# Kernel tuning notes

Measured on AMD Instinct MI355X. Metric: run time of the kernel, lower is better.

## Reference

```python
import jax, jax.numpy as jnp
import numpy as np

DK, DL, HID = 128, 128, 128  # per init_kwargs: mlp_list=[256,128,128]


def setup_inputs() -> dict:
    key = jax.random.key(0)
    k1, k2, k3, k4, k5 = jax.random.split(key, 5)
    B, K, L = 2, 128, 4096
    inputA = jax.random.normal(k1, (B, K, DK), dtype=jnp.float32)
    inputB = jax.random.normal(k2, (B, L, DL), dtype=jnp.float32)
    # MLP layer 0: Linear(256 -> 128), kaiming-uniform-ish init
    lim1 = 1.0 / np.sqrt(DK + DL)
    W1 = jax.random.uniform(k3, (DK + DL, HID), jnp.float32, -lim1, lim1)
    b1 = jax.random.uniform(k4, (HID,), jnp.float32, -lim1, lim1)
    # scoring Linear(128 -> 1, bias=False)
    lim2 = 1.0 / np.sqrt(HID)
    w2 = jax.random.uniform(k5, (HID,), jnp.float32, -lim2, lim2)
    return {"inputA": inputA, "inputB": inputB, "W1": W1, "b1": b1,
            "w2": w2, "nA": K, "nB": L}


def reference(inputA, inputB, W1, b1, w2, nA, nB):
    # Original: tC = cat([repeat(A), repeat(B)], -1); mlp(tC); linear; softmax(L).
    # Fused-equivalent math: split W1 rows between the A-part and B-part of the
    # concat, so the first Linear is two small matmuls + broadcast add.
    hA = jnp.einsum('bkd,dh->bkh', inputA, W1[:DK])        # (B, K, H)
    hB = jnp.einsum('bld,dh->blh', inputB, W1[DK:])        # (B, L, H)
    h = jax.nn.relu(hA[:, :, None, :] + hB[:, None, :, :] + b1)  # (B, K, L, H)
    scores = jnp.einsum('bklh,h->bkl', h, w2)              # (B, K, L)
    return jax.nn.softmax(scores, axis=2)
```

## Files before the change

### kernel.cpp

```cpp
#include <hip/hip_runtime.h>
#include <hip/hip_fp16.h>
#include <math.h>

constexpr int BB = 2;
constexpr int KK = 128;
constexpr int LL = 4096;
constexpr int DD = 128;
constexpr int HH = 128;

__device__ __forceinline__ float4 ld4(const float* p) {
    return *reinterpret_cast<const float4*>(p);
}

__device__ __forceinline__ __half2 hmax2(__half2 a, __half2 b) {
    unsigned ua = __builtin_bit_cast(unsigned, a);
    unsigned ub = __builtin_bit_cast(unsigned, b);
    unsigned ud;
    asm("v_pk_max_f16 %0, %1, %2" : "=v"(ud) : "v"(ua), "v"(ub));
    return __builtin_bit_cast(__half2, ud);
}

__device__ __forceinline__ uint32_t duph(float x) {
    __half h = __float2half(x);
    unsigned short us = __builtin_bit_cast(unsigned short, h);
    return (uint32_t)us * 0x10001u;
}

__global__ __launch_bounds__(256) void k1_gemm(
    const float* __restrict__ inA, const float* __restrict__ inB,
    const float* __restrict__ W1, const float* __restrict__ b1,
    const float* __restrict__ w2,
    uint32_t* __restrict__ u_dup, uint32_t* __restrict__ w2_dup,
    __half* __restrict__ vT)
{
    __shared__ __align__(16) char smem[49 * 1024];
    float*  sIn = reinterpret_cast<float*>(smem);
    float4* sW4 = reinterpret_cast<float4*>(smem + 16 * 1024);
    float*  sT  = reinterpret_cast<float*>(smem + 16 * 1024);

    const int bid = blockIdx.x;
    const int tid = threadIdx.x;

    int row0;
    bool isA;
    if (bid < 256) {
        const int x = bid & 7, y = bid >> 3;
        const int C = x + 8 * (y & 1);
        row0 = C * 512 + (y >> 1) * 32;
        isA = false;
    } else {
        row0 = (bid - 256) * 32;
        isA = true;
    }
    const float* src = (isA ? inA : inB) + (size_t)row0 * DD;
    const float4* wsrc = reinterpret_cast<const float4*>(W1 + (isA ? 0 : DD * HH));

    #pragma unroll
    for (int j = 0; j < 4; ++j) {
        const int idx = tid + 256 * j;
        reinterpret_cast<float4*>(sIn)[idx] =
            reinterpret_cast<const float4*>(src)[idx];
    }

    const int tx = tid & 31;
    const int ty = tid >> 5;

    float accx[4], accy[4], accz[4], accw[4];
    #pragma unroll
    for (int r = 0; r < 4; ++r) { accx[r] = accy[r] = accz[r] = accw[r] = 0.f; }

    for (int wh = 0; wh < 2; ++wh) {
        __syncthreads();
        #pragma unroll
        for (int q = 0; q < 8; ++q)
            sW4[tid + 256 * q] = wsrc[wh * 2048 + tid + 256 * q];
        __syncthreads();

        #pragma unroll 2
        for (int dd0 = 0; dd0 < 64; dd0 += 4) {
            const int d0 = wh * 64 + dd0;
            float4 w4[4];
            #pragma unroll
            for (int dd = 0; dd < 4; ++dd)
                w4[dd] = sW4[(dd0 + dd) * 32 + tx];
            float a[4][4];
            #pragma unroll
            for (int r = 0; r < 4; ++r) {
                float4 a4 = ld4(&sIn[(ty * 4 + r) * 128 + d0]);
                a[r][0] = a4.x; a[r][1] = a4.y; a[r][2] = a4.z; a[r][3] = a4.w;
            }
            #pragma unroll
            for (int dd = 0; dd < 4; ++dd) {
                const float4 wv = w4[dd];
                #pragma unroll
                for (int r = 0; r < 4; ++r) {
                    const float av = a[r][dd];
                    accx[r] = fmaf(av, wv.x, accx[r]);
                    accy[r] = fmaf(av, wv.y, accy[r]);
                    accz[r] = fmaf(av, wv.z, accz[r]);
                    accw[r] = fmaf(av, wv.w, accw[r]);
                }
            }
        }
    }

    if (isA) {
        const float4 bb = ld4(&b1[tx * 4]);
        #pragma unroll
        for (int r = 0; r < 4; ++r) {
            uint4 o;
            o.x = duph(accx[r] + bb.x);
            o.y = duph(accy[r] + bb.y);
            o.z = duph(accz[r] + bb.z);
            o.w = duph(accw[r] + bb.w);
            *reinterpret_cast<uint4*>(
                &u_dup[(size_t)(row0 + ty * 4 + r) * HH + tx * 4]) = o;
        }
        if (bid == 256 && tid < HH) w2_dup[tid] = duph(w2[tid]);
    } else {
        __syncthreads();
        #pragma unroll
        for (int r = 0; r < 4; ++r) {
            const int l = ty * 4 + r;
            sT[(tx * 4 + 0) * 33 + l] = accx[r];
            sT[(tx * 4 + 1) * 33 + l] = accy[r];
            sT[(tx * 4 + 2) * 33 + l] = accz[r];
            sT[(tx * 4 + 3) * 33 + l] = accw[r];
        }
        __syncthreads();
        const int h    = tid >> 1;
        const int half = tid & 1;
        const int bsel = row0 >> 12;
        const int l0   = (row0 & 4095) + half * 16;
        uint32_t o[8];
        #pragma unroll
        for (int i = 0; i < 8; ++i) {
            const float lo = sT[h * 33 + half * 16 + 2 * i];
            const float hi = sT[h * 33 + half * 16 + 2 * i + 1];
            o[i] = __builtin_bit_cast(uint32_t, __floats2half2_rn(lo, hi));
        }
        uint32_t* dst = reinterpret_cast<uint32_t*>(vT) +
                        (size_t)(bsel * HH + h) * (LL / 2) + l0 / 2;
        uint4 s0; s0.x = o[0]; s0.y = o[1]; s0.z = o[2]; s0.w = o[3];
        uint4 s1; s1.x = o[4]; s1.y = o[5]; s1.z = o[6]; s1.w = o[7];
        *reinterpret_cast<uint4*>(dst)     = s0;
        *reinterpret_cast<uint4*>(dst + 4) = s1;
    }
}

__global__ __launch_bounds__(512) void k2_score(
    const uint32_t* __restrict__ u_dup, const uint32_t* __restrict__ w2_dup,
    const __half* __restrict__ vT, float* __restrict__ out)
{
    __shared__ __align__(16) uint32_t sU[8 * HH];
    __shared__ __align__(16) uint32_t sW[HH];

    int m = blockIdx.x;
    const int cb = m & 7;   m >>= 3;
    const int kt = m & 15;  m >>= 4;
    const int b  = m;
    const int tid = threadIdx.x;

    if (tid < 256)
        reinterpret_cast<uint4*>(sU)[tid] =
            reinterpret_cast<const uint4*>(u_dup + (size_t)(b * KK + kt * 8) * HH)[tid];
    else if (tid < 288)
        reinterpret_cast<uint4*>(sW)[tid - 256] =
            reinterpret_cast<const uint4*>(w2_dup)[tid - 256];
    __syncthreads();

    const int kh = tid >> 8;
    const int t  = tid & 255;
    const int p  = cb * 256 + t;
    const uint32_t* vp = reinterpret_cast<const uint32_t*>(vT)
                         + (size_t)b * HH * (LL / 2) + p;
    const uint32_t* su = sU + kh * 4 * HH;

    const __half2 hz = __float2half2_rn(0.f);
    float2 facc[4];
    #pragma unroll
    for (int k = 0; k < 4; ++k) { facc[k].x = 0.f; facc[k].y = 0.f; }

    for (int g = 0; g < 8; ++g) {
        const int h0 = g * 16;
        uint32_t v[16];
        #pragma unroll
        for (int jj = 0; jj < 16; ++jj)
            v[jj] = vp[(size_t)(h0 + jj) * (LL / 2)];

        __half2 acc[4];
        #pragma unroll
        for (int k = 0; k < 4; ++k) acc[k] = hz;

        #pragma unroll
        for (int q = 0; q < 4; ++q) {
            const uint4 wc = *reinterpret_cast<const uint4*>(&sW[h0 + q * 4]);
            uint4 uc[4];
            #pragma unroll
            for (int k = 0; k < 4; ++k)
                uc[k] = *reinterpret_cast<const uint4*>(&su[k * HH + h0 + q * 4]);
            const uint32_t* wq = reinterpret_cast<const uint32_t*>(&wc);
            #pragma unroll
            for (int jj = 0; jj < 4; ++jj) {
                const __half2 ww = __builtin_bit_cast(__half2, wq[jj]);
                const __half2 vv = __builtin_bit_cast(__half2, v[q * 4 + jj]);
                #pragma unroll
                for (int k = 0; k < 4; ++k) {
                    const uint32_t* uq = reinterpret_cast<const uint32_t*>(&uc[k]);
                    __half2 tt = __hadd2(vv, __builtin_bit_cast(__half2, uq[jj]));
                    acc[k] = __hfma2(hmax2(tt, hz), ww, acc[k]);
                }
            }
        }
        #pragma unroll
        for (int k = 0; k < 4; ++k) {
            const float2 f = __half22float2(acc[k]);
            facc[k].x += f.x; facc[k].y += f.y;
        }
    }

    #pragma unroll
    for (int k = 0; k < 4; ++k)
        *reinterpret_cast<float2*>(
            &out[(size_t)(b * KK + kt * 8 + kh * 4 + k) * LL + 2 * p]) = facc[k];
}

__global__ __launch_bounds__(1024) void k3_softmax(float* __restrict__ out)
{
    __shared__ float reds[16];

    const int row = blockIdx.x;
    float* p = out + (size_t)row * LL;
    const int tid = threadIdx.x;

    float4 x = reinterpret_cast<const float4*>(p)[tid];

    x.x = expf(x.x); x.y = expf(x.y);
    x.z = expf(x.z); x.w = expf(x.w);
    float s = (x.x + x.y) + (x.z + x.w);
    #pragma unroll
    for (int off = 32; off > 0; off >>= 1)
        s += __shfl_xor(s, off, 64);
    const int lane = tid & 63, wv = tid >> 6;
    if (lane == 0) reds[wv] = s;
    __syncthreads();
    if (tid < 16) {
        float ss = reds[tid];
        #pragma unroll
        for (int off = 8; off > 0; off >>= 1)
            ss += __shfl_xor(ss, off, 64);
        reds[tid] = ss;
    }
    __syncthreads();
    s = reds[0];

    const float inv = 1.0f / s;
    x.x *= inv; x.y *= inv; x.z *= inv; x.w *= inv;
    reinterpret_cast<float4*>(p)[tid] = x;
}

extern "C" void kernel_launch(void* const* d_in, const int* in_sizes, int n_in,
                              void* d_out, int out_size, void* d_ws, size_t ws_size,
                              hipStream_t stream)
{
    const float* inA = (const float*)d_in[0];
    const float* inB = (const float*)d_in[1];
    const float* W1  = (const float*)d_in[2];
    const float* b1  = (const float*)d_in[3];
    const float* w2  = (const float*)d_in[4];
    float* out = (float*)d_out;

    char* ws = (char*)d_ws;
    uint32_t* u_dup  = (uint32_t*)ws;
    uint32_t* w2_dup = (uint32_t*)(ws + 0x20000);
    __half*   vT     = (__half*)(ws + 0x40000);

    hipLaunchKernelGGL(k1_gemm, dim3(264), dim3(256), 0, stream,
                       inA, inB, W1, b1, w2, u_dup, w2_dup, vT);
    hipLaunchKernelGGL(k2_score, dim3(256), dim3(512), 0, stream,
                       u_dup, w2_dup, vT, out);
    hipLaunchKernelGGL(k3_softmax, dim3(BB * KK), dim3(1024), 0, stream, out);
}
```

Measured before the change: 30.19 us.

## Pack hidden dim as half2 pairs and read per-thread hB rows

Changes the packed-half layout so each half2 holds two hidden channels instead of two L positions. hB is now stored row-major (L,H) in fp16 with no shared-memory transpose, and the duplicated u/w2 buffers become compact packed pairs. The score kernel gives each thread one L position and 8 K rows, loads its 256-byte hB row with vector loads, and reads u and w2 straight from global memory (uniform, likely scalar loads) instead of staging them in LDS. The aim is to drop the transpose and LDS traffic and halve the u/w2 footprint. In exchange, row-per-thread loads are strided across lanes, which may coalesce poorly, and the output stores become scalar.

```diff
diff --git a/kernel.cpp b/kernel.cpp
--- a/kernel.cpp
+++ b/kernel.cpp
@@ -20,23 +20,20 @@
     return __builtin_bit_cast(__half2, ud);
 }
 
-__device__ __forceinline__ uint32_t duph(float x) {
-    __half h = __float2half(x);
-    unsigned short us = __builtin_bit_cast(unsigned short, h);
-    return (uint32_t)us * 0x10001u;
+__device__ __forceinline__ uint32_t pkh2(float a, float b) {
+    return __builtin_bit_cast(uint32_t, __floats2half2_rn(a, b));
 }
 
 __global__ __launch_bounds__(256) void k1_gemm(
     const float* __restrict__ inA, const float* __restrict__ inB,
     const float* __restrict__ W1, const float* __restrict__ b1,
     const float* __restrict__ w2,
-    uint32_t* __restrict__ u_dup, uint32_t* __restrict__ w2_dup,
-    __half* __restrict__ vT)
-{
-    __shared__ __align__(16) char smem[49 * 1024];
+    uint32_t* __restrict__ u_pk, uint32_t* __restrict__ w2_pk,
+    __half* __restrict__ vh)
+{
+    __shared__ __align__(16) char smem[48 * 1024];
     float*  sIn = reinterpret_cast<float*>(smem);
     float4* sW4 = reinterpret_cast<float4*>(smem + 16 * 1024);
-    float*  sT  = reinterpret_cast<float*>(smem + 16 * 1024);
 
     const int bid = blockIdx.x;
     const int tid = threadIdx.x;
@@ -108,121 +105,80 @@
         const float4 bb = ld4(&b1[tx * 4]);
         #pragma unroll
         for (int r = 0; r < 4; ++r) {
-            uint4 o;
-            o.x = duph(accx[r] + bb.x);
-            o.y = duph(accy[r] + bb.y);
-            o.z = duph(accz[r] + bb.z);
-            o.w = duph(accw[r] + bb.w);
-            *reinterpret_cast<uint4*>(
-                &u_dup[(size_t)(row0 + ty * 4 + r) * HH + tx * 4]) = o;
-        }
-        if (bid == 256 && tid < HH) w2_dup[tid] = duph(w2[tid]);
+            uint2 o;
+            o.x = pkh2(accx[r] + bb.x, accy[r] + bb.y);
+            o.y = pkh2(accz[r] + bb.z, accw[r] + bb.w);
+            *reinterpret_cast<uint2*>(
+                &u_pk[(size_t)(row0 + ty * 4 + r) * 64 + tx * 2]) = o;
+        }
+        if (bid == 256 && tid < 64)
+            w2_pk[tid] = pkh2(w2[2 * tid], w2[2 * tid + 1]);
     } else {
-        __syncthreads();
+        const int bsel = row0 >> 12;
         #pragma unroll
         for (int r = 0; r < 4; ++r) {
-            const int l = ty * 4 + r;
-            sT[(tx * 4 + 0) * 33 + l] = accx[r];
-            sT[(tx * 4 + 1) * 33 + l] = accy[r];
-            sT[(tx * 4 + 2) * 33 + l] = accz[r];
-            sT[(tx * 4 + 3) * 33 + l] = accw[r];
-        }
-        __syncthreads();
-        const int h    = tid >> 1;
-        const int half = tid & 1;
-        const int bsel = row0 >> 12;
-        const int l0   = (row0 & 4095) + half * 16;
-        uint32_t o[8];
-        #pragma unroll
-        for (int i = 0; i < 8; ++i) {
-            const float lo = sT[h * 33 + half * 16 + 2 * i];
-            const float hi = sT[h * 33 + half * 16 + 2 * i + 1];
-            o[i] = __builtin_bit_cast(uint32_t, __floats2half2_rn(lo, hi));
-        }
-        uint32_t* dst = reinterpret_cast<uint32_t*>(vT) +
-                        (size_t)(bsel * HH + h) * (LL / 2) + l0 / 2;
-        uint4 s0; s0.x = o[0]; s0.y = o[1]; s0.z = o[2]; s0.w = o[3];
-        uint4 s1; s1.x = o[4]; s1.y = o[5]; s1.z = o[6]; s1.w = o[7];
-        *reinterpret_cast<uint4*>(dst)     = s0;
-        *reinterpret_cast<uint4*>(dst + 4) = s1;
+            const int lrow = (row0 & 4095) + ty * 4 + r;
+            uint2 o;
+            o.x = pkh2(accx[r], accy[r]);
+            o.y = pkh2(accz[r], accw[r]);
+            *reinterpret_cast<uint2*>(
+                &vh[((size_t)bsel * LL + lrow) * HH + tx * 4]) = o;
+        }
     }
 }
 
 __global__ __launch_bounds__(512) void k2_score(
-    const uint32_t* __restrict__ u_dup, const uint32_t* __restrict__ w2_dup,
-    const __half* __restrict__ vT, float* __restrict__ out)
-{
-    __shared__ __align__(16) uint32_t sU[8 * HH];
-    __shared__ __align__(16) uint32_t sW[HH];
-
+    const uint32_t* __restrict__ u_pk, const uint32_t* __restrict__ w2_pk,
+    const __half* __restrict__ vh, float* __restrict__ out)
+{
     int m = blockIdx.x;
     const int cb = m & 7;   m >>= 3;
     const int kt = m & 15;  m >>= 4;
     const int b  = m;
     const int tid = threadIdx.x;
 
-    if (tid < 256)
-        reinterpret_cast<uint4*>(sU)[tid] =
-            reinterpret_cast<const uint4*>(u_dup + (size_t)(b * KK + kt * 8) * HH)[tid];
-    else if (tid < 288)
-        reinterpret_cast<uint4*>(sW)[tid - 256] =
-            reinterpret_cast<const uint4*>(w2_dup)[tid - 256];
-    __syncthreads();
-
-    const int kh = tid >> 8;
-    const int t  = tid & 255;
-    const int p  = cb * 256 + t;
-    const uint32_t* vp = reinterpret_cast<const uint32_t*>(vT)
-                         + (size_t)b * HH * (LL / 2) + p;
-    const uint32_t* su = sU + kh * 4 * HH;
-
+    const int l = cb * 512 + tid;
+    const uint4* vrow = reinterpret_cast<const uint4*>(
+                            vh + ((size_t)b * LL + l) * HH);
+    const uint32_t* up = u_pk + (size_t)(b * KK + kt * 8) * 64;
     const __half2 hz = __float2half2_rn(0.f);
-    float2 facc[4];
-    #pragma unroll
-    for (int k = 0; k < 4; ++k) { facc[k].x = 0.f; facc[k].y = 0.f; }
-
+
+    float acc[8];
+    #pragma unroll
+    for (int k = 0; k < 8; ++k) acc[k] = 0.f;
+
+    #pragma unroll
     for (int g = 0; g < 8; ++g) {
-        const int h0 = g * 16;
-        uint32_t v[16];
-        #pragma unroll
-        for (int jj = 0; jj < 16; ++jj)
-            v[jj] = vp[(size_t)(h0 + jj) * (LL / 2)];
-
-        __half2 acc[4];
-        #pragma unroll
-        for (int k = 0; k < 4; ++k) acc[k] = hz;
-
-        #pragma unroll
-        for (int q = 0; q < 4; ++q) {
-            const uint4 wc = *reinterpret_cast<const uint4*>(&sW[h0 + q * 4]);
-            uint4 uc[4];
-            #pragma unroll
-            for (int k = 0; k < 4; ++k)
-                uc[k] = *reinterpret_cast<const uint4*>(&su[k * HH + h0 + q * 4]);
-            const uint32_t* wq = reinterpret_cast<const uint32_t*>(&wc);
-            #pragma unroll
-            for (int jj = 0; jj < 4; ++jj) {
-                const __half2 ww = __builtin_bit_cast(__half2, wq[jj]);
-                const __half2 vv = __builtin_bit_cast(__half2, v[q * 4 + jj]);
-                #pragma unroll
-                for (int k = 0; k < 4; ++k) {
-                    const uint32_t* uq = reinterpret_cast<const uint32_t*>(&uc[k]);
-                    __half2 tt = __hadd2(vv, __builtin_bit_cast(__half2, uq[jj]));
-                    acc[k] = __hfma2(hmax2(tt, hz), ww, acc[k]);
-                }
+        const uint4 va = vrow[2 * g];
+        const uint4 vb = vrow[2 * g + 1];
+        uint32_t v[8];
+        v[0] = va.x; v[1] = va.y; v[2] = va.z; v[3] = va.w;
+        v[4] = vb.x; v[5] = vb.y; v[6] = vb.z; v[7] = vb.w;
+
+        __half2 h2[8];
+        #pragma unroll
+        for (int k = 0; k < 8; ++k) h2[k] = hz;
+
+        #pragma unroll
+        for (int k = 0; k < 8; ++k) {
+            #pragma unroll
+            for (int j = 0; j < 8; ++j) {
+                const __half2 uu = __builtin_bit_cast(__half2, up[k * 64 + g * 8 + j]);
+                const __half2 ww = __builtin_bit_cast(__half2, w2_pk[g * 8 + j]);
+                __half2 t = __hadd2(__builtin_bit_cast(__half2, v[j]), uu);
+                h2[k] = __hfma2(hmax2(t, hz), ww, h2[k]);
             }
         }
         #pragma unroll
-        for (int k = 0; k < 4; ++k) {
-            const float2 f = __half22float2(acc[k]);
-            facc[k].x += f.x; facc[k].y += f.y;
-        }
-    }
-
-    #pragma unroll
-    for (int k = 0; k < 4; ++k)
-        *reinterpret_cast<float2*>(
-            &out[(size_t)(b * KK + kt * 8 + kh * 4 + k) * LL + 2 * p]) = facc[k];
+        for (int k = 0; k < 8; ++k) {
+            const float2 f = __half22float2(h2[k]);
+            acc[k] += f.x + f.y;
+        }
+    }
+
+    #pragma unroll
+    for (int k = 0; k < 8; ++k)
+        out[(size_t)(b * KK + kt * 8 + k) * LL + l] = acc[k];
 }
 
 __global__ __launch_bounds__(1024) void k3_softmax(float* __restrict__ out)
@@ -271,13 +227,13 @@
     float* out = (float*)d_out;
 
     char* ws = (char*)d_ws;
-    uint32_t* u_dup  = (uint32_t*)ws;
-    uint32_t* w2_dup = (uint32_t*)(ws + 0x20000);
-    __half*   vT     = (__half*)(ws + 0x40000);
+    uint32_t* u_pk  = (uint32_t*)ws;
+    uint32_t* w2_pk = (uint32_t*)(ws + 0x10000);
+    __half*   vh    = (__half*)(ws + 0x20000);
 
     hipLaunchKernelGGL(k1_gemm, dim3(264), dim3(256), 0, stream,
-                       inA, inB, W1, b1, w2, u_dup, w2_dup, vT);
+                       inA, inB, W1, b1, w2, u_pk, w2_pk, vh);
     hipLaunchKernelGGL(k2_score, dim3(256), dim3(512), 0, stream,
-                       u_dup, w2_dup, vT, out);
+                       u_pk, w2_pk, vh, out);
     hipLaunchKernelGGL(k3_softmax, dim3(BB * KK), dim3(1024), 0, stream, out);
 }
```

Measured after the change: 31.39 us. +4.0%, slower.

## Store B-projection in h-group-blocked fp16 layout for vectorized score loads

Applied to the files above, without the earlier changes.

The intermediate hB tensor is now stored as [b][h-group][l-pair][16 h] packed half2, so the scoring kernel reads each 16-h group with four 128-bit loads per thread instead of sixteen strided 32-bit loads. The GEMM kernel writes this layout directly from registers, dropping the shared-memory transpose and its two barriers. The scoring inner loop is rewritten with clang vector f16 builtins in place of inline asm max, and the g loop is fully unrolled. In exchange, the GEMM stores become scattered 32-bit writes, and register pressure in the score kernel may rise.

```diff
diff --git a/kernel.cpp b/kernel.cpp
--- a/kernel.cpp
+++ b/kernel.cpp
@@ -8,16 +8,14 @@
 constexpr int DD = 128;
 constexpr int HH = 128;
 
+typedef _Float16 f16x2 __attribute__((ext_vector_type(2)));
+
 __device__ __forceinline__ float4 ld4(const float* p) {
     return *reinterpret_cast<const float4*>(p);
 }
 
-__device__ __forceinline__ __half2 hmax2(__half2 a, __half2 b) {
-    unsigned ua = __builtin_bit_cast(unsigned, a);
-    unsigned ub = __builtin_bit_cast(unsigned, b);
-    unsigned ud;
-    asm("v_pk_max_f16 %0, %1, %2" : "=v"(ud) : "v"(ua), "v"(ub));
-    return __builtin_bit_cast(__half2, ud);
+__device__ __forceinline__ uint32_t pkh2(float a, float b) {
+    return __builtin_bit_cast(uint32_t, __floats2half2_rn(a, b));
 }
 
 __device__ __forceinline__ uint32_t duph(float x) {
@@ -25,18 +23,18 @@
     unsigned short us = __builtin_bit_cast(unsigned short, h);
     return (uint32_t)us * 0x10001u;
 }
+
 
 __global__ __launch_bounds__(256) void k1_gemm(
     const float* __restrict__ inA, const float* __restrict__ inB,
     const float* __restrict__ W1, const float* __restrict__ b1,
     const float* __restrict__ w2,
     uint32_t* __restrict__ u_dup, uint32_t* __restrict__ w2_dup,
-    __half* __restrict__ vT)
-{
-    __shared__ __align__(16) char smem[49 * 1024];
+    uint32_t* __restrict__ vT2)
+{
+    __shared__ __align__(16) char smem[48 * 1024];
     float*  sIn = reinterpret_cast<float*>(smem);
     float4* sW4 = reinterpret_cast<float4*>(smem + 16 * 1024);
-    float*  sT  = reinterpret_cast<float*>(smem + 16 * 1024);
 
     const int bid = blockIdx.x;
     const int tid = threadIdx.x;
@@ -65,9 +63,11 @@
     const int tx = tid & 31;
     const int ty = tid >> 5;
 
-    float accx[4], accy[4], accz[4], accw[4];
-    #pragma unroll
-    for (int r = 0; r < 4; ++r) { accx[r] = accy[r] = accz[r] = accw[r] = 0.f; }
+    float acc[4][4];
+    #pragma unroll
+    for (int r = 0; r < 4; ++r)
+        #pragma unroll
+        for (int c = 0; c < 4; ++c) acc[r][c] = 0.f;
 
     for (int wh = 0; wh < 2; ++wh) {
         __syncthreads();
@@ -95,10 +95,10 @@
                 #pragma unroll
                 for (int r = 0; r < 4; ++r) {
                     const float av = a[r][dd];
-                    accx[r] = fmaf(av, wv.x, accx[r]);
-                    accy[r] = fmaf(av, wv.y, accy[r]);
-                    accz[r] = fmaf(av, wv.z, accz[r]);
-                    accw[r] = fmaf(av, wv.w, accw[r]);
+                    acc[r][0] = fmaf(av, wv.x, acc[r][0]);
+                    acc[r][1] = fmaf(av, wv.y, acc[r][1]);
+                    acc[r][2] = fmaf(av, wv.z, acc[r][2]);
+                    acc[r][3] = fmaf(av, wv.w, acc[r][3]);
                 }
             }
         }
@@ -106,51 +106,35 @@
 
     if (isA) {
         const float4 bb = ld4(&b1[tx * 4]);
+        const float bv[4] = { bb.x, bb.y, bb.z, bb.w };
         #pragma unroll
         for (int r = 0; r < 4; ++r) {
             uint4 o;
-            o.x = duph(accx[r] + bb.x);
-            o.y = duph(accy[r] + bb.y);
-            o.z = duph(accz[r] + bb.z);
-            o.w = duph(accw[r] + bb.w);
+            o.x = duph(acc[r][0] + bv[0]);
+            o.y = duph(acc[r][1] + bv[1]);
+            o.z = duph(acc[r][2] + bv[2]);
+            o.w = duph(acc[r][3] + bv[3]);
             *reinterpret_cast<uint4*>(
                 &u_dup[(size_t)(row0 + ty * 4 + r) * HH + tx * 4]) = o;
         }
         if (bid == 256 && tid < HH) w2_dup[tid] = duph(w2[tid]);
     } else {
-        __syncthreads();
-        #pragma unroll
-        for (int r = 0; r < 4; ++r) {
-            const int l = ty * 4 + r;
-            sT[(tx * 4 + 0) * 33 + l] = accx[r];
-            sT[(tx * 4 + 1) * 33 + l] = accy[r];
-            sT[(tx * 4 + 2) * 33 + l] = accz[r];
-            sT[(tx * 4 + 3) * 33 + l] = accw[r];
-        }
-        __syncthreads();
-        const int h    = tid >> 1;
-        const int half = tid & 1;
         const int bsel = row0 >> 12;
-        const int l0   = (row0 & 4095) + half * 16;
-        uint32_t o[8];
-        #pragma unroll
-        for (int i = 0; i < 8; ++i) {
-            const float lo = sT[h * 33 + half * 16 + 2 * i];
-            const float hi = sT[h * 33 + half * 16 + 2 * i + 1];
-            o[i] = __builtin_bit_cast(uint32_t, __floats2half2_rn(lo, hi));
-        }
-        uint32_t* dst = reinterpret_cast<uint32_t*>(vT) +
-                        (size_t)(bsel * HH + h) * (LL / 2) + l0 / 2;
-        uint4 s0; s0.x = o[0]; s0.y = o[1]; s0.z = o[2]; s0.w = o[3];
-        uint4 s1; s1.x = o[4]; s1.y = o[5]; s1.z = o[6]; s1.w = o[7];
-        *reinterpret_cast<uint4*>(dst)     = s0;
-        *reinterpret_cast<uint4*>(dst + 4) = s1;
+        const int lp0  = ((row0 & 4095) + ty * 4) >> 1;
+        uint32_t* vb = vT2 + (size_t)bsel * (8 * 2048 * 16);
+        #pragma unroll
+        for (int c = 0; c < 4; ++c) {
+            const int h = tx * 4 + c, g = h >> 4, ph = h & 15;
+            uint32_t* dst = vb + ((size_t)g * 2048 + lp0) * 16 + ph;
+            dst[0]  = pkh2(acc[0][c], acc[1][c]);
+            dst[16] = pkh2(acc[2][c], acc[3][c]);
+        }
     }
 }
 
 __global__ __launch_bounds__(512) void k2_score(
     const uint32_t* __restrict__ u_dup, const uint32_t* __restrict__ w2_dup,
-    const __half* __restrict__ vT, float* __restrict__ out)
+    const uint32_t* __restrict__ vT2, float* __restrict__ out)
 {
     __shared__ __align__(16) uint32_t sU[8 * HH];
     __shared__ __align__(16) uint32_t sW[HH];
@@ -171,58 +155,59 @@
 
     const int kh = tid >> 8;
     const int t  = tid & 255;
-    const int p  = cb * 256 + t;
-    const uint32_t* vp = reinterpret_cast<const uint32_t*>(vT)
-                         + (size_t)b * HH * (LL / 2) + p;
-    const uint32_t* su = sU + kh * 4 * HH;
-
-    const __half2 hz = __float2half2_rn(0.f);
+    const int lp = cb * 256 + t;
+
+    const uint4* vg = reinterpret_cast<const uint4*>(
+                          vT2 + ((size_t)b * 8 * 2048 + lp) * 16);
+    const uint4* su4 = reinterpret_cast<const uint4*>(sU + kh * 4 * HH);
+    const uint4* sw4 = reinterpret_cast<const uint4*>(sW);
+
+    const f16x2 hz = { (_Float16)0, (_Float16)0 };
     float2 facc[4];
     #pragma unroll
     for (int k = 0; k < 4; ++k) { facc[k].x = 0.f; facc[k].y = 0.f; }
 
+    #pragma unroll
     for (int g = 0; g < 8; ++g) {
-        const int h0 = g * 16;
-        uint32_t v[16];
-        #pragma unroll
-        for (int jj = 0; jj < 16; ++jj)
-            v[jj] = vp[(size_t)(h0 + jj) * (LL / 2)];
-
-        __half2 acc[4];
-        #pragma unroll
-        for (int k = 0; k < 4; ++k) acc[k] = hz;
-
-        #pragma unroll
-        for (int q = 0; q < 4; ++q) {
-            const uint4 wc = *reinterpret_cast<const uint4*>(&sW[h0 + q * 4]);
-            uint4 uc[4];
-            #pragma unroll
-            for (int k = 0; k < 4; ++k)
-                uc[k] = *reinterpret_cast<const uint4*>(&su[k * HH + h0 + q * 4]);
-            const uint32_t* wq = reinterpret_cast<const uint32_t*>(&wc);
-            #pragma unroll
-            for (int jj = 0; jj < 4; ++jj) {
-                const __half2 ww = __builtin_bit_cast(__half2, wq[jj]);
-                const __half2 vv = __builtin_bit_cast(__half2, v[q * 4 + jj]);
-                #pragma unroll
-                for (int k = 0; k < 4; ++k) {
-                    const uint32_t* uq = reinterpret_cast<const uint32_t*>(&uc[k]);
-                    __half2 tt = __hadd2(vv, __builtin_bit_cast(__half2, uq[jj]));
-                    acc[k] = __hfma2(hmax2(tt, hz), ww, acc[k]);
-                }
+        uint4 vq[4];
+        #pragma unroll
+        for (int c = 0; c < 4; ++c)
+            vq[c] = vg[(size_t)g * 8192 + c];
+        const uint32_t* vd = reinterpret_cast<const uint32_t*>(vq);
+
+        uint4 wq[4];
+        #pragma unroll
+        for (int c = 0; c < 4; ++c) wq[c] = sw4[g * 4 + c];
+        const uint32_t* wd = reinterpret_cast<const uint32_t*>(wq);
+
+        f16x2 hacc[4] = { hz, hz, hz, hz };
+        #pragma unroll
+        for (int k = 0; k < 4; ++k) {
+            uint4 uq[4];
+            #pragma unroll
+            for (int c = 0; c < 4; ++c) uq[c] = su4[k * 32 + g * 4 + c];
+            const uint32_t* ud = reinterpret_cast<const uint32_t*>(uq);
+            #pragma unroll
+            for (int ph = 0; ph < 16; ++ph) {
+                f16x2 vv = __builtin_bit_cast(f16x2, vd[ph]);
+                f16x2 uu = __builtin_bit_cast(f16x2, ud[ph]);
+                f16x2 ww = __builtin_bit_cast(f16x2, wd[ph]);
+                f16x2 s = vv + uu;
+                s = __builtin_elementwise_max(s, hz);
+                hacc[k] = s * ww + hacc[k];
             }
         }
         #pragma unroll
         for (int k = 0; k < 4; ++k) {
-            const float2 f = __half22float2(acc[k]);
-            facc[k].x += f.x; facc[k].y += f.y;
+            facc[k].x += (float)hacc[k].x;
+            facc[k].y += (float)hacc[k].y;
         }
     }
 
     #pragma unroll
     for (int k = 0; k < 4; ++k)
         *reinterpret_cast<float2*>(
-            &out[(size_t)(b * KK + kt * 8 + kh * 4 + k) * LL + 2 * p]) = facc[k];
+            &out[(size_t)(b * KK + kt * 8 + kh * 4 + k) * LL + 2 * lp]) = facc[k];
 }
 
 __global__ __launch_bounds__(1024) void k3_softmax(float* __restrict__ out)
@@ -273,11 +258,11 @@
     char* ws = (char*)d_ws;
     uint32_t* u_dup  = (uint32_t*)ws;
     uint32_t* w2_dup = (uint32_t*)(ws + 0x20000);
-    __half*   vT     = (__half*)(ws + 0x40000);
+    uint32_t* vT2    = (uint32_t*)(ws + 0x40000);
 
     hipLaunchKernelGGL(k1_gemm, dim3(264), dim3(256), 0, stream,
-                       inA, inB, W1, b1, w2, u_dup, w2_dup, vT);
+                       inA, inB, W1, b1, w2, u_dup, w2_dup, vT2);
     hipLaunchKernelGGL(k2_score, dim3(256), dim3(512), 0, stream,
-                       u_dup, w2_dup, vT, out);
+                       u_dup, w2_dup, vT2, out);
     hipLaunchKernelGGL(k3_softmax, dim3(BB * KK), dim3(1024), 0, stream, out);
 }
```

Measured after the change: 28.40 us. 1.06x faster.
